# Optimization experiments

Hardware: AMD Instinct MI355X
Metric: run time of the kernel (lower is better)

Reference implementation:

```python
import jax, jax.numpy as jnp
import numpy as np

B, N, D, E, DFF, CAP = 8, 2048, 1024, 8, 4096, 320


def setup_inputs() -> dict:
    key = jax.random.key(0)
    k1, k2, k3, k4 = jax.random.split(key, 4)
    return {
        "token_inputs": jax.random.normal(k1, (B, N, D), dtype=jnp.float32),
        "Wg": jax.random.normal(k2, (D, E), dtype=jnp.float32) * 0.02,
        "W1": jax.random.normal(k3, (E, D, DFF), dtype=jnp.float32) * 0.02,
        "W2": jax.random.normal(k4, (E, DFF, D), dtype=jnp.float32) * 0.02,
        "capacity": CAP,
    }


def _switch_route(token_inputs, Wg, capacity):
    # Top-1 switch routing -> dispatch one-hot [B,N,E,C], combine = dispatch * gate prob.
    logits = jnp.einsum('bnd,de->bne', token_inputs, Wg)
    probs = jax.nn.softmax(logits, axis=-1)
    gate = jnp.max(probs, axis=-1)                      # [B,N]
    expert_idx = jnp.argmax(probs, axis=-1)             # [B,N]
    mask = jax.nn.one_hot(expert_idx, probs.shape[-1], dtype=probs.dtype)  # [B,N,E]
    # 1-indexed position of each token within its chosen expert's queue
    pos = jnp.cumsum(mask, axis=1) * mask               # [B,N,E]
    mask = mask * (pos <= capacity)                     # drop tokens over capacity
    slot = (pos - 1.0).astype(jnp.int32)                # -1 where unrouted -> one_hot zeros
    dispatch = jax.nn.one_hot(slot, capacity, dtype=probs.dtype) * mask[..., None]  # [B,N,E,C]
    combine = dispatch * gate[:, :, None, None]
    return dispatch, combine


def reference(token_inputs, Wg, W1, W2, capacity):
    dispatch, combine = _switch_route(token_inputs, Wg, capacity)
    # Dispatch tokens to expert buffers: [B,E,C,D]
    expert_inputs = jnp.einsum('bnd,bnec->becd', token_inputs, dispatch)
    # Per-expert 2-layer relu FFN (grouped GEMM over E)
    h = jax.nn.relu(jnp.einsum('becd,edh->bech', expert_inputs, W1))
    expert_outputs = jnp.einsum('bech,ehd->becd', h, W2)
    # Combine back to token order, weighted by gate prob
    return jnp.einsum('becd,bnec->bnd', expert_outputs, combine)
```

## Files before the change

### kernel.cpp

```cpp
#include <hip/hip_runtime.h>

#define Bq 8
#define Nq 2048
#define Dq 1024
#define Eq 8
#define DFFq 4096
#define CAPq 320
#define Mq (Bq * CAPq)
#define Tq (Bq * Nq)

typedef __attribute__((ext_vector_type(8))) short bf16x8;
typedef __attribute__((ext_vector_type(4))) float f32x4;

static __device__ __forceinline__ unsigned short f2bf(float f) {
    union { float f; unsigned u; } v;
    v.f = f;
    unsigned r = v.u + 0x7fffu + ((v.u >> 16) & 1u);
    return (unsigned short)(r >> 16);
}

static __device__ __forceinline__ void gload_lds16(const void* g, void* l) {
    __builtin_amdgcn_global_load_lds(
        (const __attribute__((address_space(1))) unsigned int*)g,
        (__attribute__((address_space(3))) unsigned int*)l, 16, 0, 0);
}

__global__ __launch_bounds__(256) void route_kernel(
    const float* __restrict__ tok, const float* __restrict__ Wg,
    int* __restrict__ eidx, float* __restrict__ gate)
{
    int wv = threadIdx.x >> 6, lane = threadIdx.x & 63;
    int t = blockIdx.x * 4 + wv;
    const float* tp = tok + (size_t)t * Dq;
    float acc[8] = {0.f,0.f,0.f,0.f,0.f,0.f,0.f,0.f};
    for (int it = 0; it < Dq / 64; ++it) {
        int d = it * 64 + lane;
        float x = tp[d];
        const float4* w = (const float4*)(Wg + (size_t)d * 8);
        float4 w0 = w[0], w1 = w[1];
        acc[0] += x * w0.x; acc[1] += x * w0.y; acc[2] += x * w0.z; acc[3] += x * w0.w;
        acc[4] += x * w1.x; acc[5] += x * w1.y; acc[6] += x * w1.z; acc[7] += x * w1.w;
    }
#pragma unroll
    for (int e = 0; e < 8; ++e)
#pragma unroll
        for (int off = 32; off; off >>= 1)
            acc[e] += __shfl_xor(acc[e], off, 64);
    if (lane == 0) {
        float m = acc[0]; int bi = 0;
#pragma unroll
        for (int e = 1; e < 8; ++e) if (acc[e] > m) { m = acc[e]; bi = e; }
        float s = 0.f;
#pragma unroll
        for (int e = 0; e < 8; ++e) s += expf(acc[e] - m);
        eidx[t] = bi;
        gate[t] = 1.0f / s;
    }
}

__global__ __launch_bounds__(64) void slot_kernel(
    const int* __restrict__ eidx, int* __restrict__ tfs)
{
    int b = blockIdx.x >> 3, e = blockIdx.x & 7;
    int lane = threadIdx.x;
    const int* ip = eidx + (size_t)b * Nq;
    int base = (e * Bq + b) * CAPq;
    int cnt = 0;
    for (int it = 0; it < Nq / 64; ++it) {
        int n = it * 64 + lane;
        bool my = (ip[n] == e);
        unsigned long long mask = __ballot(my);
        if (my) {
            int pos = cnt + __popcll(mask & ((1ull << lane) - 1ull));
            if (pos < CAPq) tfs[base + pos] = b * Nq + n;
        }
        cnt += __popcll(mask);
    }
}

__global__ __launch_bounds__(128) void dispatch_kernel(
    const float* __restrict__ tok, const int* __restrict__ tfs,
    unsigned short* __restrict__ X)
{
    int r = blockIdx.x;
    int t = tfs[r];
    int d0 = threadIdx.x * 8;
    unsigned short o[8];
    if (t < 0) {
#pragma unroll
        for (int k = 0; k < 8; ++k) o[k] = 0;
    } else {
        const float4* p = (const float4*)(tok + (size_t)t * Dq + d0);
        float4 a = p[0], b = p[1];
        o[0]=f2bf(a.x); o[1]=f2bf(a.y); o[2]=f2bf(a.z); o[3]=f2bf(a.w);
        o[4]=f2bf(b.x); o[5]=f2bf(b.y); o[6]=f2bf(b.z); o[7]=f2bf(b.w);
    }
    *(uint4*)(X + (size_t)r * Dq + d0) = *(const uint4*)o;
}

__global__ __launch_bounds__(256) void transpose_cvt(
    const float* __restrict__ in, unsigned short* __restrict__ out,
    int R, int C)
{
    __shared__ float tile[32][33];
    int e = blockIdx.z;
    int c0 = blockIdx.x * 32, r0 = blockIdx.y * 32;
    int tx = threadIdx.x & 31, ty = threadIdx.x >> 5;
    const float* ip = in + (size_t)e * R * C;
#pragma unroll
    for (int rr = 0; rr < 4; ++rr)
        tile[ty + rr * 8][tx] = ip[(size_t)(r0 + ty + rr * 8) * C + c0 + tx];
    __syncthreads();
    unsigned short* op = out + (size_t)e * R * C;
#pragma unroll
    for (int rr = 0; rr < 4; ++rr)
        op[(size_t)(c0 + ty + rr * 8) * R + r0 + tx] = f2bf(tile[tx][ty + rr * 8]);
}

template <int MODE, int Ndim, int Kdim>
__global__ __launch_bounds__(512, 2) void gemm8p(
    const unsigned short* __restrict__ A,
    const unsigned short* __restrict__ Bt,
    unsigned short* __restrict__ Hout,
    float* __restrict__ Out,
    const int* __restrict__ tfs,
    const float* __restrict__ gate)
{
    constexpr int NKT = Kdim / 64;
    constexpr int NI  = NKT / 2;
    constexpr int NTB = Ndim / 256;
    constexpr int MT  = Mq / 256;
    constexpr int NWG = MT * NTB * Eq;

    __shared__ __align__(16) unsigned short As[2 * 2 * 128 * 64];
    __shared__ __align__(16) unsigned short Bs[2 * 2 * 128 * 64];
    __shared__ int   t_lds[256];
    __shared__ float g_lds[256];

    int flat = blockIdx.x;
    int wg = (flat & 7) * (NWG / 8) + (flat >> 3);
    int e   = wg / (MT * NTB);
    int rem = wg - e * (MT * NTB);
    int mb = rem / NTB, nb = rem - mb * NTB;
    int m0 = mb * 256, n0 = nb * 256;

    const char* Ae = (const char*)(A  + (size_t)e * Mq * Kdim + (size_t)m0 * Kdim);
    const char* Be = (const char*)(Bt + (size_t)e * Ndim * Kdim + (size_t)n0 * Kdim);

    const int tid = threadIdx.x;
    if (MODE == 1 && tid < 256) {
        int t = tfs[e * Mq + m0 + tid];
        t_lds[tid] = t;
        g_lds[tid] = (t >= 0) ? gate[t] : 0.f;
    }
    __syncthreads();

    const int lane = tid & 63;
    const int wv = tid >> 6;
    const int wr = wv & 1, wc = wv >> 1;
    const int lrow = lane & 15;
    const int lk = lane >> 4;
    const int swz = (lane & 7) << 4;

    const int sk = ((tid & 7) << 4) ^ (((tid >> 3) & 7) << 4);
    const size_t Kb = (size_t)Kdim * 2;
    const char* gA = Ae + (size_t)(tid >> 3) * Kb + sk;
    const char* gB = Be + (size_t)(tid >> 3) * Kb + sk;
    const int ldst = wv << 10;

    #define STG(gbase, lds, buf, h, kt) {                                      \
        const char* _g = (gbase) + (size_t)((h) * 128) * Kb + (size_t)(kt) * 128; \
        char* _l = (char*)(lds) + ((buf) * 2 + (h)) * 16384 + ldst;             \
        gload_lds16(_g,                   _l);                                  \
        gload_lds16(_g + (size_t)64 * Kb, _l + 8192); }

    bf16x8 aq[4][2];
    bf16x8 bq[2][2][2];
    f32x4  acc[2][2][4][2] = {};

    #define LDA(buf, mi) {                                                      \
        const char* _p = (const char*)As + ((buf) * 2 + (mi)) * 16384;          \
        _Pragma("unroll")                                                       \
        for (int i = 0; i < 4; ++i) {                                           \
            int rh = wr * 64 + i * 16 + lrow;                                   \
            aq[i][0] = *(const bf16x8*)(_p + rh * 128 + ((lk * 16) ^ swz));     \
            aq[i][1] = *(const bf16x8*)(_p + rh * 128 + ((64 + lk * 16) ^ swz)); } }

    #define LDB(buf, nj) {                                                      \
        const char* _p = (const char*)Bs + ((buf) * 2 + (nj)) * 16384;          \
        _Pragma("unroll")                                                       \
        for (int j = 0; j < 2; ++j) {                                           \
            int rh = wc * 32 + j * 16 + lrow;                                   \
            bq[nj][j][0] = *(const bf16x8*)(_p + rh * 128 + ((lk * 16) ^ swz)); \
            bq[nj][j][1] = *(const bf16x8*)(_p + rh * 128 + ((64 + lk * 16) ^ swz)); } }

    #define MM(mi, nj)                                                          \
        _Pragma("unroll")                                                       \
        for (int i = 0; i < 4; ++i)                                             \
        _Pragma("unroll")                                                       \
        for (int j = 0; j < 2; ++j)                                             \
        _Pragma("unroll")                                                       \
        for (int kk = 0; kk < 2; ++kk)                                          \
            acc[mi][nj][i][j] = __builtin_amdgcn_mfma_f32_16x16x32_bf16(        \
                aq[i][kk], bq[nj][j][kk], acc[mi][nj][i][j], 0, 0, 0);

    #define PH_BAR() { __builtin_amdgcn_s_barrier(); __builtin_amdgcn_sched_barrier(0); }
    #define LGKM0()  { asm volatile("s_waitcnt lgkmcnt(0)"); __builtin_amdgcn_sched_barrier(0); }
    #define PRIO_MM(mi, nj) { __builtin_amdgcn_s_setprio(1); MM(mi, nj); __builtin_amdgcn_s_setprio(0); }

    STG(gA, As, 0, 0, 0);
    STG(gB, Bs, 0, 0, 0);
    STG(gA, As, 0, 1, 0);
    STG(gB, Bs, 0, 1, 0);
    STG(gA, As, 1, 0, 1);
    STG(gB, Bs, 1, 0, 1);
    asm volatile("s_waitcnt vmcnt(4)");
    PH_BAR();

    for (int u = 0; u < NI; ++u) {
        const int kt0 = 2 * u, kt1 = 2 * u + 1;
        const bool lastI = (u == NI - 1);

        LDA(0, 0); LDB(0, 0);
        STG(gA, As, 1, 1, kt1);
        PH_BAR(); LGKM0(); PRIO_MM(0, 0); PH_BAR();

        LDB(0, 1);
        STG(gB, Bs, 1, 1, kt1);
        PH_BAR(); LGKM0(); PRIO_MM(0, 1); PH_BAR();

        LDA(0, 1);
        if (!lastI) STG(gA, As, 0, 0, kt0 + 2);
        PH_BAR(); LGKM0(); PRIO_MM(1, 0); PH_BAR();

        if (!lastI) STG(gB, Bs, 0, 0, kt0 + 2);
        PH_BAR(); LGKM0(); PRIO_MM(1, 1);
        if (lastI) { asm volatile("s_waitcnt vmcnt(0)"); }
        else       { asm volatile("s_waitcnt vmcnt(4)"); }
        PH_BAR();

        LDA(1, 0); LDB(1, 0);
        if (!lastI) STG(gA, As, 0, 1, kt0 + 2);
        PH_BAR(); LGKM0(); PRIO_MM(0, 0); PH_BAR();

        LDB(1, 1);
        if (!lastI) STG(gB, Bs, 0, 1, kt0 + 2);
        PH_BAR(); LGKM0(); PRIO_MM(0, 1); PH_BAR();

        LDA(1, 1);
        if (!lastI) STG(gA, As, 1, 0, kt1 + 2);
        PH_BAR(); LGKM0(); PRIO_MM(1, 0); PH_BAR();

        if (!lastI) STG(gB, Bs, 1, 0, kt1 + 2);
        PH_BAR(); LGKM0(); PRIO_MM(1, 1);
        if (!lastI) {
            asm volatile("s_waitcnt vmcnt(4)");
            PH_BAR();
        }
    }

    if (MODE == 0) {
        unsigned short* Hp = Hout + (size_t)e * Mq * Ndim;
#pragma unroll
        for (int mi = 0; mi < 2; ++mi)
#pragma unroll
        for (int nj = 0; nj < 2; ++nj)
#pragma unroll
        for (int i = 0; i < 4; ++i) {
            int row = m0 + mi * 128 + wr * 64 + i * 16 + lk * 4;
#pragma unroll
            for (int j = 0; j < 2; ++j) {
                int col = n0 + nj * 128 + wc * 32 + j * 16 + lrow;
#pragma unroll
                for (int r = 0; r < 4; ++r)
                    Hp[(size_t)(row + r) * Ndim + col] =
                        f2bf(fmaxf(acc[mi][nj][i][j][r], 0.f));
            }
        }
    } else {
#pragma unroll
        for (int mi = 0; mi < 2; ++mi)
#pragma unroll
        for (int i = 0; i < 4; ++i) {
            int rl = mi * 128 + wr * 64 + i * 16 + lk * 4;
#pragma unroll
            for (int r = 0; r < 4; ++r) {
                int tt = t_lds[rl + r];
                if (tt < 0) continue;
                float g = g_lds[rl + r];
#pragma unroll
                for (int nj = 0; nj < 2; ++nj)
#pragma unroll
                for (int j = 0; j < 2; ++j) {
                    int col = n0 + nj * 128 + wc * 32 + j * 16 + lrow;
                    Out[(size_t)tt * Dq + col] = g * acc[mi][nj][i][j][r];
                }
            }
        }
    }
    #undef STG
    #undef LDA
    #undef LDB
    #undef MM
    #undef PH_BAR
    #undef LGKM0
    #undef PRIO_MM
}

extern "C" void kernel_launch(void* const* d_in, const int* in_sizes, int n_in,
                              void* d_out, int out_size, void* d_ws, size_t ws_size,
                              hipStream_t stream)
{
    const float* tok = (const float*)d_in[0];
    const float* Wg  = (const float*)d_in[1];
    const float* W1  = (const float*)d_in[2];
    const float* W2  = (const float*)d_in[3];
    float* out = (float*)d_out;
    char* ws = (char*)d_ws;

    unsigned short* W1T = (unsigned short*)(ws);
    unsigned short* W2T = (unsigned short*)(ws + 67108864);
    unsigned short* X   = (unsigned short*)(ws + 134217728);
    unsigned short* H   = (unsigned short*)(ws + 176160768);
    int*   tfs  = (int*)(ws + 343932928);
    int*   eidx = (int*)(ws + 344014848);
    float* gate = (float*)(ws + 344080384);

    hipMemsetAsync(d_out, 0, (size_t)out_size * 4, stream);
    hipMemsetAsync(tfs, 0xFF, Eq * Mq * 4, stream);

    route_kernel<<<Tq / 4, 256, 0, stream>>>(tok, Wg, eidx, gate);
    slot_kernel<<<Bq * Eq, 64, 0, stream>>>(eidx, tfs);
    dispatch_kernel<<<Eq * Mq, 128, 0, stream>>>(tok, tfs, X);
    transpose_cvt<<<dim3(DFFq / 32, Dq / 32, Eq), 256, 0, stream>>>(W1, W1T, Dq, DFFq);
    transpose_cvt<<<dim3(Dq / 32, DFFq / 32, Eq), 256, 0, stream>>>(W2, W2T, DFFq, Dq);

    gemm8p<0, DFFq, Dq><<<(Mq / 256) * (DFFq / 256) * Eq, 512, 0, stream>>>(
        X, W1T, H, nullptr, nullptr, nullptr);
    gemm8p<1, Dq, DFFq><<<(Mq / 256) * (Dq / 256) * Eq, 512, 0, stream>>>(
        H, W2T, nullptr, out, tfs, gate);
}
```

Measured before the change: 572.8 us.

## Restructure GEMM main loop into register double-buffered B fragments with fewer barriers

Rewrites the expert GEMM K-loop so B fragments alternate between two register sets and the LDS reads for the next quadrant are issued before the current MFMA block runs. It drops the per-phase lgkmcnt(0) waits and half the barriers, interleaving global-to-LDS staging with MFMAs under raised priority, and peels the final iteration into a separate epilogue. The aim is to hide LDS read latency and cut barrier stalls, at the cost of more VGPR pressure and a more fragile hand-tuned schedule with vmcnt counts that must match the staging order.

```diff
diff --git a/kernel.cpp b/kernel.cpp
--- a/kernel.cpp
+++ b/kernel.cpp
@@ -168,14 +168,14 @@
     const char* gB = Be + (size_t)(tid >> 3) * Kb + sk;
     const int ldst = wv << 10;
 
-    #define STG(gbase, lds, buf, h, kt) {                                      \
+    #define STG(gbase, lds, buf, h, kt) {                                       \
         const char* _g = (gbase) + (size_t)((h) * 128) * Kb + (size_t)(kt) * 128; \
-        char* _l = (char*)(lds) + ((buf) * 2 + (h)) * 16384 + ldst;             \
-        gload_lds16(_g,                   _l);                                  \
+        char* _l = (char*)(lds) + ((buf) * 2 + (h)) * 16384 + ldst;              \
+        gload_lds16(_g,                   _l);                                   \
         gload_lds16(_g + (size_t)64 * Kb, _l + 8192); }
 
     bf16x8 aq[4][2];
-    bf16x8 bq[2][2][2];
+    bf16x8 bq0[2][2], bq1[2][2];
     f32x4  acc[2][2][4][2] = {};
 
     #define LDA(buf, mi) {                                                      \
@@ -186,77 +186,100 @@
             aq[i][0] = *(const bf16x8*)(_p + rh * 128 + ((lk * 16) ^ swz));     \
             aq[i][1] = *(const bf16x8*)(_p + rh * 128 + ((64 + lk * 16) ^ swz)); } }
 
-    #define LDB(buf, nj) {                                                      \
-        const char* _p = (const char*)Bs + ((buf) * 2 + (nj)) * 16384;          \
+    #define LDB(bqz, buf, h) {                                                  \
+        const char* _p = (const char*)Bs + ((buf) * 2 + (h)) * 16384;           \
         _Pragma("unroll")                                                       \
         for (int j = 0; j < 2; ++j) {                                           \
             int rh = wc * 32 + j * 16 + lrow;                                   \
-            bq[nj][j][0] = *(const bf16x8*)(_p + rh * 128 + ((lk * 16) ^ swz)); \
-            bq[nj][j][1] = *(const bf16x8*)(_p + rh * 128 + ((64 + lk * 16) ^ swz)); } }
-
-    #define MM(mi, nj)                                                          \
+            bqz[j][0] = *(const bf16x8*)(_p + rh * 128 + ((lk * 16) ^ swz));    \
+            bqz[j][1] = *(const bf16x8*)(_p + rh * 128 + ((64 + lk * 16) ^ swz)); } }
+
+    #define MMQ(mi, bqz, z)                                                     \
         _Pragma("unroll")                                                       \
         for (int i = 0; i < 4; ++i)                                             \
         _Pragma("unroll")                                                       \
         for (int j = 0; j < 2; ++j)                                             \
         _Pragma("unroll")                                                       \
         for (int kk = 0; kk < 2; ++kk)                                          \
-            acc[mi][nj][i][j] = __builtin_amdgcn_mfma_f32_16x16x32_bf16(        \
-                aq[i][kk], bq[nj][j][kk], acc[mi][nj][i][j], 0, 0, 0);
-
-    #define PH_BAR() { __builtin_amdgcn_s_barrier(); __builtin_amdgcn_sched_barrier(0); }
-    #define LGKM0()  { asm volatile("s_waitcnt lgkmcnt(0)"); __builtin_amdgcn_sched_barrier(0); }
-    #define PRIO_MM(mi, nj) { __builtin_amdgcn_s_setprio(1); MM(mi, nj); __builtin_amdgcn_s_setprio(0); }
+            acc[mi][z][i][j] = __builtin_amdgcn_mfma_f32_16x16x32_bf16(         \
+                aq[i][kk], bqz[j][kk], acc[mi][z][i][j], 0, 0, 0);
+
+    #define SB __builtin_amdgcn_sched_barrier(0)
+    #define BAR { __builtin_amdgcn_s_barrier(); SB; }
+    #define VM(n) { asm volatile("s_waitcnt vmcnt(" #n ")"); SB; }
+    #define P1 __builtin_amdgcn_s_setprio(1)
+    #define P0 __builtin_amdgcn_s_setprio(0)
 
     STG(gA, As, 0, 0, 0);
     STG(gB, Bs, 0, 0, 0);
+    STG(gB, Bs, 0, 1, 0);
     STG(gA, As, 0, 1, 0);
-    STG(gB, Bs, 0, 1, 0);
     STG(gA, As, 1, 0, 1);
-    STG(gB, Bs, 1, 0, 1);
-    asm volatile("s_waitcnt vmcnt(4)");
-    PH_BAR();
-
-    for (int u = 0; u < NI; ++u) {
-        const int kt0 = 2 * u, kt1 = 2 * u + 1;
-        const bool lastI = (u == NI - 1);
-
-        LDA(0, 0); LDB(0, 0);
-        STG(gA, As, 1, 1, kt1);
-        PH_BAR(); LGKM0(); PRIO_MM(0, 0); PH_BAR();
-
-        LDB(0, 1);
-        STG(gB, Bs, 1, 1, kt1);
-        PH_BAR(); LGKM0(); PRIO_MM(0, 1); PH_BAR();
-
-        LDA(0, 1);
-        if (!lastI) STG(gA, As, 0, 0, kt0 + 2);
-        PH_BAR(); LGKM0(); PRIO_MM(1, 0); PH_BAR();
-
-        if (!lastI) STG(gB, Bs, 0, 0, kt0 + 2);
-        PH_BAR(); LGKM0(); PRIO_MM(1, 1);
-        if (lastI) { asm volatile("s_waitcnt vmcnt(0)"); }
-        else       { asm volatile("s_waitcnt vmcnt(4)"); }
-        PH_BAR();
-
-        LDA(1, 0); LDB(1, 0);
-        if (!lastI) STG(gA, As, 0, 1, kt0 + 2);
-        PH_BAR(); LGKM0(); PRIO_MM(0, 0); PH_BAR();
-
-        LDB(1, 1);
-        if (!lastI) STG(gB, Bs, 0, 1, kt0 + 2);
-        PH_BAR(); LGKM0(); PRIO_MM(0, 1); PH_BAR();
-
-        LDA(1, 1);
-        if (!lastI) STG(gA, As, 1, 0, kt1 + 2);
-        PH_BAR(); LGKM0(); PRIO_MM(1, 0); PH_BAR();
-
-        if (!lastI) STG(gB, Bs, 1, 0, kt1 + 2);
-        PH_BAR(); LGKM0(); PRIO_MM(1, 1);
-        if (!lastI) {
-            asm volatile("s_waitcnt vmcnt(4)");
-            PH_BAR();
-        }
+    VM(6); BAR;
+    LDB(bq0, 0, 0);
+    LDA(0, 0);
+    SB;
+    VM(4); BAR;
+
+    for (int u = 0; u < NI - 1; ++u) {
+        const int ktb1 = 2 * u + 1, ktb0n = 2 * u + 2, ktb1n = 2 * u + 3;
+        LDB(bq1, 0, 1); SB;
+        STG(gB, Bs, 1, 0, ktb1);
+        P1; MMQ(0, bq0, 0); P0;
+        VM(4); BAR;
+        STG(gB, Bs, 1, 1, ktb1);
+        P1; MMQ(0, bq1, 1); P0;
+        LDA(0, 1); SB;
+        BAR;
+        STG(gA, As, 1, 1, ktb1);
+        P1; MMQ(1, bq0, 0); P0;
+        VM(4); BAR;
+        LDB(bq0, 1, 0); SB;
+        STG(gA, As, 0, 0, ktb0n);
+        P1; MMQ(1, bq1, 1); P0;
+        LDA(1, 0); SB;
+        VM(4); BAR;
+        LDB(bq1, 1, 1); SB;
+        STG(gB, Bs, 0, 0, ktb0n);
+        P1; MMQ(0, bq0, 0); P0;
+        VM(4); BAR;
+        STG(gB, Bs, 0, 1, ktb0n);
+        P1; MMQ(0, bq1, 1); P0;
+        LDA(1, 1); SB;
+        BAR;
+        STG(gA, As, 0, 1, ktb0n);
+        P1; MMQ(1, bq0, 0); P0;
+        VM(4); BAR;
+        LDB(bq0, 0, 0); SB;
+        STG(gA, As, 1, 0, ktb1n);
+        P1; MMQ(1, bq1, 1); P0;
+        LDA(0, 0); SB;
+        VM(4); BAR;
+    }
+
+    {
+        LDB(bq1, 0, 1); SB;
+        STG(gB, Bs, 1, 0, NKT - 1);
+        P1; MMQ(0, bq0, 0); P0;
+        VM(4); BAR;
+        STG(gB, Bs, 1, 1, NKT - 1);
+        P1; MMQ(0, bq1, 1); P0;
+        LDA(0, 1); SB;
+        BAR;
+        STG(gA, As, 1, 1, NKT - 1);
+        P1; MMQ(1, bq0, 0); P0;
+        VM(4); BAR;
+        LDB(bq0, 1, 0); SB;
+        P1; MMQ(1, bq1, 1); P0;
+        LDA(1, 0); SB;
+        VM(2); BAR;
+        LDB(bq1, 1, 1); SB;
+        P1; MMQ(0, bq0, 0); P0;
+        VM(0); BAR;
+        P1; MMQ(0, bq1, 1); P0;
+        LDA(1, 1); SB;
+        P1; MMQ(1, bq0, 0); P0;
+        P1; MMQ(1, bq1, 1); P0;
     }
 
     if (MODE == 0) {
@@ -301,10 +324,12 @@
     #undef STG
     #undef LDA
     #undef LDB
-    #undef MM
-    #undef PH_BAR
-    #undef LGKM0
-    #undef PRIO_MM
+    #undef MMQ
+    #undef SB
+    #undef BAR
+    #undef VM
+    #undef P1
+    #undef P0
 }
 
 extern "C" void kernel_launch(void* const* d_in, const int* in_sizes, int n_in,
```

Measured after the change: 562.3 us. Within noise of the previous version (-1.8%).
